# Kernel tuning notes

Measured on AMD Instinct MI355X. Metric: run time of the kernel, lower is better.

Reference implementation:

```python
import jax, jax.numpy as jnp
import numpy as np

B, T, E, D, A = 32, 2048, 1024, 1024, 1024
SHARPENING = 1.0


def setup_inputs() -> dict:
    key = jax.random.key(0)
    ks = jax.random.split(key, 8)
    s = 0.02
    return {
        "enc_out": jax.random.normal(ks[0], (B, T, E), jnp.float32),
        "x_lens": jax.random.randint(ks[1], (B,), 1, T + 1, jnp.int32),
        "dec_out": jax.random.normal(ks[2], (B, 1, D), jnp.float32),
        "att_weights_step": jax.random.uniform(ks[3], (B, T), jnp.float32),
        "W_enc": jax.random.normal(ks[4], (E, A), jnp.float32) * s,
        "b_enc": jnp.zeros((A,), jnp.float32),
        "W_dec": jax.random.normal(ks[5], (D, A), jnp.float32) * s,
        "v": jax.random.normal(ks[6], (A,), jnp.float32) * s,
    }


def reference(enc_out, x_lens, dec_out, att_weights_step, W_enc, b_enc, W_dec, v):
    # content (Bahdanau additive) attention
    # energy[b,t] = v . tanh(W_enc enc[b,t] + b_enc + W_dec dec[b])
    enc_proj = jnp.einsum("bte,ea->bta", enc_out, W_enc) + b_enc  # [B,T,A]
    dec_proj = jnp.einsum("bod,da->boa", dec_out, W_dec)          # [B,1,A]
    energy = jnp.einsum("bta,a->bt", jnp.tanh(enc_proj + dec_proj), v)  # [B,T]
    # original multiplies energy by a 0/1 length mask (NOT -inf masking)
    mask = (jnp.arange(T)[None, :] < x_lens[:, None]).astype(energy.dtype)
    energy = energy * mask * SHARPENING
    att = jax.nn.softmax(energy, axis=-1)  # [B,T]
    context_vec = jnp.einsum("bte,bt->be", enc_out, att)[:, None, :]  # [B,1,E]
    return context_vec, att
```

## Files before the change

### kernel.cpp

```cpp
#include <hip/hip_runtime.h>
#include <hip/hip_bf16.h>
#include <stdint.h>


typedef __bf16 bf16;
typedef __bf16 bf16x8 __attribute__((ext_vector_type(8)));
typedef __bf16 bf16x4 __attribute__((ext_vector_type(4)));
typedef float floatx4 __attribute__((ext_vector_type(4)));

#define T_DIM 2048
#define B_DIM 32
#define K_DIM 1024
#define N_DIM 1024
#define M_DIM (B_DIM * T_DIM)
#define ENC_ELEMS ((size_t)M_DIM * K_DIM)

__device__ __forceinline__ void async_copy16(const bf16* g, bf16* l) {
    __builtin_amdgcn_global_load_lds(
        (const __attribute__((address_space(1))) void*)g,
        (__attribute__((address_space(3))) void*)l, 16, 0, 0);
}

__device__ __forceinline__ float fast_tanh(float x) {
    float ax = fabsf(x);
    float e  = __expf(ax + ax);
    float t  = 1.f - 2.f / (e + 1.f);
    return copysignf(t, x);
}

__global__ __launch_bounds__(256) void cvt_enc(const float* __restrict__ in,
                                               bf16* __restrict__ out) {
    size_t i = ((size_t)blockIdx.x * 256 + threadIdx.x) * 8;
    const size_t stride = (size_t)gridDim.x * 256 * 8;
    for (; i < ENC_ELEMS; i += stride) {
        float4 f0 = *(const float4*)(in + i);
        float4 f1 = *(const float4*)(in + i + 4);
        bf16x8 w;
        w[0] = (bf16)f0.x; w[1] = (bf16)f0.y; w[2] = (bf16)f0.z; w[3] = (bf16)f0.w;
        w[4] = (bf16)f1.x; w[5] = (bf16)f1.y; w[6] = (bf16)f1.z; w[7] = (bf16)f1.w;
        *(bf16x8*)(out + i) = w;
    }
}

__global__ __launch_bounds__(256) void transpose_wenc(
        const float* __restrict__ W, bf16* __restrict__ WT) {
    __shared__ bf16 tile[64][65];
    const int e0 = blockIdx.x * 64, a0 = blockIdx.y * 64;
    const int c = threadIdx.x & 63, r0 = threadIdx.x >> 6;
#pragma unroll
    for (int p = 0; p < 16; ++p) {
        int r = p * 4 + r0;
        tile[r][c] = (bf16)W[(size_t)(e0 + r) * 1024 + a0 + c];
    }
    __syncthreads();
#pragma unroll
    for (int p = 0; p < 16; ++p) {
        int r = p * 4 + r0;
        WT[(size_t)(a0 + r) * 1024 + e0 + c] = tile[c][r];
    }
}

__global__ __launch_bounds__(256) void decproj_kernel(
        const float* __restrict__ dec, const float* __restrict__ Wdec,
        const float* __restrict__ benc, float* __restrict__ dproj) {
    const int bg = blockIdx.x;
    const int a0 = blockIdx.y * 64;
    const int al = threadIdx.x & 63;
    const int dq = threadIdx.x >> 6;
    const int a  = a0 + al;
    __shared__ float sdec[8][1024];
    for (int i = threadIdx.x; i < 8192; i += 256)
        sdec[i >> 10][i & 1023] = dec[bg * 8192 + i];
    __syncthreads();
    float acc[8];
#pragma unroll
    for (int b = 0; b < 8; ++b) acc[b] = 0.f;
    for (int d = dq * 256; d < dq * 256 + 256; ++d) {
        const float w = Wdec[(size_t)d * 1024 + a];
#pragma unroll
        for (int b = 0; b < 8; ++b) acc[b] += sdec[b][d] * w;
    }
    __shared__ float red[4][8][64];
#pragma unroll
    for (int b = 0; b < 8; ++b) red[dq][b][al] = acc[b];
    __syncthreads();
    if (dq == 0) {
        const float be = benc[a];
#pragma unroll
        for (int b = 0; b < 8; ++b)
            dproj[(bg * 8 + b) * 1024 + a] =
                be + red[0][b][al] + red[1][b][al] + red[2][b][al] + red[3][b][al];
    }
}


#define HT 8192

#define BARRIER()  __builtin_amdgcn_s_barrier()
#define SCHEDB()   __builtin_amdgcn_sched_barrier(0)
#define VMCNT(n)   asm volatile("s_waitcnt vmcnt(" #n ")")

#define STAGE_A(kt, h) {                                                       \
    const bf16* g_ = encb + (size_t)(m0 + (h)*128 + wave*8 + (lane>>3)) * 1024 \
                     + (kt)*64 + srccol;                                       \
    bf16* l_ = As + ((((kt)&1)*2 + (h)) * HT) + wave * 512;                    \
    async_copy16(g_, l_);                                                      \
    async_copy16(g_ + (size_t)64*1024, l_ + 4096);                             \
}
#define STAGE_B(kt, h) {                                                       \
    const bf16* g_ = WT + (size_t)(n0 + (h)*128 + wave*8 + (lane>>3)) * 1024   \
                     + (kt)*64 + srccol;                                       \
    bf16* l_ = Bs + ((((kt)&1)*2 + (h)) * HT) + wave * 512;                    \
    async_copy16(g_, l_);                                                      \
    async_copy16(g_ + (size_t)64*1024, l_ + 4096);                             \
}

#define PHASE(tt, qm, qn, RA, STAGECODE, WAITCODE) {                           \
    const bf16* Ah_ = As + (((tt) & 1) * 2 + (qm)) * HT;                       \
    const bf16* Bh_ = Bs + (((tt) & 1) * 2 + (qn)) * HT;                       \
    if (RA) {                                                                  \
      _Pragma("unroll") for (int mf_ = 0; mf_ < 4; ++mf_) {                    \
        afr[mf_][0] = *(const bf16x8*)(Ah_ + (wm*64 + mf_*16 + lo)*64 + swz0); \
        afr[mf_][1] = *(const bf16x8*)(Ah_ + (wm*64 + mf_*16 + lo)*64 + swz1); \
      }                                                                        \
    }                                                                          \
    _Pragma("unroll") for (int nf_ = 0; nf_ < 2; ++nf_) {                      \
      bfr[nf_][0] = *(const bf16x8*)(Bh_ + (wn*32 + nf_*16 + lo)*64 + swz0);   \
      bfr[nf_][1] = *(const bf16x8*)(Bh_ + (wn*32 + nf_*16 + lo)*64 + swz1);   \
    }                                                                          \
    STAGECODE;                                                                 \
    SCHEDB();                                                                  \
    BARRIER();                                                                 \
    SCHEDB();                                                                  \
    __builtin_amdgcn_s_setprio(1);                                             \
    _Pragma("unroll") for (int kk_ = 0; kk_ < 2; ++kk_)                        \
      _Pragma("unroll") for (int mf_ = 0; mf_ < 4; ++mf_)                      \
        _Pragma("unroll") for (int nf_ = 0; nf_ < 2; ++nf_)                    \
          acc[qm][qn][mf_][nf_] = __builtin_amdgcn_mfma_f32_16x16x32_bf16(     \
              afr[mf_][kk_], bfr[nf_][kk_], acc[qm][qn][mf_][nf_], 0, 0, 0);   \
    __builtin_amdgcn_s_setprio(0);                                             \
    SCHEDB();                                                                  \
    WAITCODE;                                                                  \
    SCHEDB();                                                                  \
    BARRIER();                                                                 \
    SCHEDB();                                                                  \
}

__global__ __launch_bounds__(512, 2) void energy_gemm_8ph(
        const bf16* __restrict__ encb, const bf16* __restrict__ WT,
        const float* __restrict__ dproj, const float* __restrict__ v,
        float* __restrict__ part) {
    __shared__ __align__(16) bf16 As[4 * HT];
    __shared__ __align__(16) bf16 Bs[4 * HT];
    __shared__ float esum[4 * 256];

    const int tid  = threadIdx.x;
    const int lane = tid & 63;
    const int wave = tid >> 6;
    const int wm   = wave >> 2;
    const int wn   = wave & 3;
    const int lo   = lane & 15;
    const int hi   = lane >> 4;

    const int L = blockIdx.x;
    const int xcd  = L & 7;
    const int slot = L >> 3;
    const int m_tile  = xcd * 32 + (slot >> 2);
    const int n_chunk = slot & 3;
    const int m0 = m_tile * 256;
    const int n0 = n_chunk * 256;
    const int b  = m0 >> 11;

    const int srccol = (((lane & 7) ^ (lane >> 3)) << 3);
    const int swz0 = ((hi)     ^ (lo & 7)) << 3;
    const int swz1 = ((4 | hi) ^ (lo & 7)) << 3;

    floatx4 acc[2][2][4][2];
#pragma unroll
    for (int a_ = 0; a_ < 2; ++a_)
#pragma unroll
      for (int b_ = 0; b_ < 2; ++b_)
#pragma unroll
        for (int c_ = 0; c_ < 4; ++c_)
#pragma unroll
          for (int d_ = 0; d_ < 2; ++d_)
            acc[a_][b_][c_][d_] = (floatx4){0.f, 0.f, 0.f, 0.f};

    bf16x8 afr[4][2], bfr[2][2];

    float vv[2][2], dp[2][2];
#pragma unroll
    for (int qn = 0; qn < 2; ++qn)
#pragma unroll
      for (int nf = 0; nf < 2; ++nf) {
        int col = n0 + qn * 128 + wn * 32 + nf * 16 + lo;
        vv[qn][nf] = v[col];
        dp[qn][nf] = dproj[b * 1024 + col];
      }
    SCHEDB();
    VMCNT(0);
    SCHEDB();

    STAGE_A(0, 0); STAGE_B(0, 0); STAGE_A(0, 1); STAGE_B(0, 1);
    STAGE_A(1, 0); STAGE_B(1, 0);
    SCHEDB();
    VMCNT(4);
    SCHEDB();
    BARRIER();
    SCHEDB();

#pragma unroll 1
    for (int i = 0; i < 7; ++i) {
        const int t0 = 2 * i, t1 = t0 + 1, t2 = t0 + 2, t3 = t0 + 3;
        PHASE(t0, 0, 0, 1, { STAGE_A(t1, 1); }, {});
        PHASE(t0, 0, 1, 0, { STAGE_B(t1, 1); }, {});
        PHASE(t0, 1, 0, 1, { STAGE_A(t2, 0); }, {});
        PHASE(t0, 1, 1, 0, { STAGE_B(t2, 0); }, { VMCNT(4); });
        PHASE(t1, 0, 0, 1, { STAGE_A(t2, 1); }, {});
        PHASE(t1, 0, 1, 0, { STAGE_B(t2, 1); }, {});
        PHASE(t1, 1, 0, 1, { STAGE_A(t3, 0); }, {});
        PHASE(t1, 1, 1, 0, { STAGE_B(t3, 0); }, { VMCNT(4); });
    }
    PHASE(14, 0, 0, 1, { STAGE_A(15, 1); }, {});
    PHASE(14, 0, 1, 0, { STAGE_B(15, 1); }, {});
    PHASE(14, 1, 0, 1, {}, {});
    PHASE(14, 1, 1, 0, {}, { VMCNT(0); });
    PHASE(15, 0, 0, 1, {}, {});
    PHASE(15, 0, 1, 0, {}, {});
    PHASE(15, 1, 0, 1, {}, {});
    PHASE(15, 1, 1, 0, {}, {});

#pragma unroll
    for (int qm = 0; qm < 2; ++qm)
#pragma unroll
      for (int mf = 0; mf < 4; ++mf)
#pragma unroll
        for (int r = 0; r < 4; ++r) {
          float s = 0.f;
#pragma unroll
          for (int qn = 0; qn < 2; ++qn)
#pragma unroll
            for (int nf = 0; nf < 2; ++nf)
              s += vv[qn][nf] * fast_tanh(acc[qm][qn][mf][nf][r] + dp[qn][nf]);
          s += __shfl_xor(s, 1);
          s += __shfl_xor(s, 2);
          s += __shfl_xor(s, 4);
          s += __shfl_xor(s, 8);
          if (lo == 0)
            esum[wn * 256 + qm * 128 + wm * 64 + mf * 16 + hi * 4 + r] = s;
        }
    __syncthreads();
    if (tid < 256)
        part[(size_t)n_chunk * M_DIM + m0 + tid] =
            esum[tid] + esum[256 + tid] + esum[512 + tid] + esum[768 + tid];
}

__global__ __launch_bounds__(256) void energy_gemm_f32(
        const float* __restrict__ enc, const bf16* __restrict__ WT,
        const float* __restrict__ dproj, const float* __restrict__ v,
        float* __restrict__ part) {
    __shared__ __align__(16) bf16 As[128 * 32];
    __shared__ __align__(16) bf16 Bs[128 * 32];
    __shared__ float esum[128];

    const int tid  = threadIdx.x;
    const int lane = tid & 63;
    const int wave = tid >> 6;
    const int wy = wave >> 1, wx = wave & 1;
    const int L = blockIdx.x;
    const int xcd  = L & 7;
    const int slot = L >> 3;
    const int m_tile = xcd * 64 + (slot >> 3);
    const int n_chunk = slot & 7;
    const int m0 = m_tile * 128;
    const int n0 = n_chunk * 128;
    const int b  = m0 >> 11;

    if (tid < 128) esum[tid] = 0.f;

    floatx4 acc[4][4];
#pragma unroll
    for (int i = 0; i < 4; ++i)
#pragma unroll
        for (int j = 0; j < 4; ++j) acc[i][j] = (floatx4){0.f, 0.f, 0.f, 0.f};

    const int sr = tid >> 2;
    const int sc = (tid & 3) * 8;
    const float* gA = enc + (size_t)(m0 + sr) * 1024 + sc;
    const bf16*  gB = WT  + (size_t)(n0 + sr) * 1024 + sc;
    bf16* lA = As + sr * 32 + sc;
    bf16* lB = Bs + sr * 32 + sc;

    for (int k0 = 0; k0 < K_DIM; k0 += 32) {
        __syncthreads();
#pragma unroll
        for (int rep = 0; rep < 2; ++rep) {
            const float4* p = (const float4*)(gA + (size_t)rep * 64 * 1024 + k0);
            float4 f0 = p[0], f1 = p[1];
            bf16x8 w;
            w[0] = (bf16)f0.x; w[1] = (bf16)f0.y; w[2] = (bf16)f0.z; w[3] = (bf16)f0.w;
            w[4] = (bf16)f1.x; w[5] = (bf16)f1.y; w[6] = (bf16)f1.z; w[7] = (bf16)f1.w;
            *(bf16x8*)(lA + rep * 64 * 32) = w;
            *(bf16x8*)(lB + rep * 64 * 32) =
                *(const bf16x8*)(gB + (size_t)rep * 64 * 1024 + k0);
        }
        __syncthreads();

        bf16x8 af[4], bfrg[4];
#pragma unroll
        for (int i = 0; i < 4; ++i)
            af[i] = *(const bf16x8*)(As + (wy * 64 + i * 16 + (lane & 15)) * 32 + (lane >> 4) * 8);
#pragma unroll
        for (int i = 0; i < 4; ++i)
            bfrg[i] = *(const bf16x8*)(Bs + (wx * 64 + i * 16 + (lane & 15)) * 32 + (lane >> 4) * 8);
#pragma unroll
        for (int mi = 0; mi < 4; ++mi)
#pragma unroll
            for (int ni = 0; ni < 4; ++ni)
                acc[mi][ni] = __builtin_amdgcn_mfma_f32_16x16x32_bf16(
                    af[mi], bfrg[ni], acc[mi][ni], 0, 0, 0);
    }
    __syncthreads();

    float vv[4], dp[4];
#pragma unroll
    for (int ni = 0; ni < 4; ++ni) {
        int col = n0 + wx * 64 + ni * 16 + (lane & 15);
        vv[ni] = v[col];
        dp[ni] = dproj[b * 1024 + col];
    }
#pragma unroll
    for (int mi = 0; mi < 4; ++mi) {
#pragma unroll
        for (int r = 0; r < 4; ++r) {
            float s = 0.f;
#pragma unroll
            for (int ni = 0; ni < 4; ++ni)
                s += vv[ni] * fast_tanh(acc[mi][ni][r] + dp[ni]);
            s += __shfl_xor(s, 1);
            s += __shfl_xor(s, 2);
            s += __shfl_xor(s, 4);
            s += __shfl_xor(s, 8);
            if ((lane & 15) == 0) {
                int row = wy * 64 + mi * 16 + (lane >> 4) * 4 + r;
                atomicAdd(&esum[row], s);
            }
        }
    }
    __syncthreads();
    if (tid < 128) part[(size_t)n_chunk * M_DIM + m0 + tid] = esum[tid];
}

__global__ __launch_bounds__(256) void softmax_kernel(
        const float* __restrict__ part, const int* __restrict__ xlens,
        float* __restrict__ att, int nc) {
    const int b = blockIdx.x, tid = threadIdx.x;
    const int len = xlens[b];
    float e[8];
    float mx = -3.4e38f;
#pragma unroll
    for (int i = 0; i < 8; ++i) {
        const int t = tid + i * 256;
        float s = 0.f;
#pragma unroll 4
        for (int c = 0; c < nc; ++c) s += part[(size_t)c * M_DIM + b * 2048 + t];
        e[i] = (t < len) ? s : 0.f;
        mx = fmaxf(mx, e[i]);
    }
#pragma unroll
    for (int off = 1; off < 64; off <<= 1) mx = fmaxf(mx, __shfl_xor(mx, off));
    __shared__ float sr1[4], sr2[4];
    if ((tid & 63) == 0) sr1[tid >> 6] = mx;
    __syncthreads();
    mx = fmaxf(fmaxf(sr1[0], sr1[1]), fmaxf(sr1[2], sr1[3]));
    float sum = 0.f;
#pragma unroll
    for (int i = 0; i < 8; ++i) { e[i] = __expf(e[i] - mx); sum += e[i]; }
#pragma unroll
    for (int off = 1; off < 64; off <<= 1) sum += __shfl_xor(sum, off);
    if ((tid & 63) == 0) sr2[tid >> 6] = sum;
    __syncthreads();
    sum = sr2[0] + sr2[1] + sr2[2] + sr2[3];
    const float inv = 1.f / sum;
#pragma unroll
    for (int i = 0; i < 8; ++i)
        att[b * 2048 + tid + i * 256] = e[i] * inv;
}

__global__ __launch_bounds__(256) void context_part_kernel(
        const bf16* __restrict__ encb, const float* __restrict__ att,
        float* __restrict__ ctxpart) {
    const int b = blockIdx.x, chunk = blockIdx.y, tid = threadIdx.x;
    const int t0 = chunk * 128;
    __shared__ float satt[128];
    if (tid < 128) satt[tid] = att[b * 2048 + t0 + tid];
    __syncthreads();
    const bf16* base = encb + ((size_t)b * 2048 + t0) * 1024 + tid * 4;
    float a0 = 0.f, a1 = 0.f, a2 = 0.f, a3 = 0.f;
#pragma unroll 4
    for (int t = 0; t < 128; ++t) {
        bf16x4 ev = *(const bf16x4*)(base + (size_t)t * 1024);
        float w = satt[t];
        a0 += w * (float)ev[0]; a1 += w * (float)ev[1];
        a2 += w * (float)ev[2]; a3 += w * (float)ev[3];
    }
    float* o = ctxpart + ((size_t)b * 16 + chunk) * 1024 + tid * 4;
    o[0] = a0; o[1] = a1; o[2] = a2; o[3] = a3;
}

__global__ __launch_bounds__(256) void context_reduce_kernel(
        const float* __restrict__ ctxpart, float* __restrict__ out_ctx) {
    const int i = blockIdx.x * 256 + threadIdx.x;
    const int b = i >> 10, e = i & 1023;
    const float* p = ctxpart + (size_t)b * 16 * 1024 + e;
    float s = 0.f;
#pragma unroll
    for (int c = 0; c < 16; ++c) s += p[c * 1024];
    out_ctx[i] = s;
}

__global__ __launch_bounds__(256) void context_kernel_f32(
        const float* __restrict__ enc, const float* __restrict__ att,
        float* __restrict__ ctx) {
    const int b = blockIdx.x, t0 = blockIdx.y * 128, tid = threadIdx.x;
    __shared__ float satt[128];
    if (tid < 128) satt[tid] = att[b * 2048 + t0 + tid];
    __syncthreads();
    const float* base = enc + ((size_t)b * 2048 + t0) * 1024 + tid * 4;
    float a0 = 0.f, a1 = 0.f, a2 = 0.f, a3 = 0.f;
    for (int t = 0; t < 128; ++t) {
        float4 ev = *(const float4*)(base + (size_t)t * 1024);
        float w = satt[t];
        a0 += w * ev.x; a1 += w * ev.y; a2 += w * ev.z; a3 += w * ev.w;
    }
    float* o = ctx + b * 1024 + tid * 4;
    atomicAdd(o + 0, a0); atomicAdd(o + 1, a1);
    atomicAdd(o + 2, a2); atomicAdd(o + 3, a3);
}

extern "C" void kernel_launch(void* const* d_in, const int* in_sizes, int n_in,
                              void* d_out, int out_size, void* d_ws, size_t ws_size,
                              hipStream_t stream) {
    const float* enc   = (const float*)d_in[0];
    const int*   xlens = (const int*)d_in[1];
    const float* dec   = (const float*)d_in[2];
    const float* Wenc  = (const float*)d_in[4];
    const float* benc  = (const float*)d_in[5];
    const float* Wdec  = (const float*)d_in[6];
    const float* v     = (const float*)d_in[7];

    float* out_ctx = (float*)d_out;
    float* out_att = out_ctx + B_DIM * K_DIM;

    char* ws = (char*)d_ws;
    float* dproj   = (float*)ws;
    bf16*  WT      = (bf16*)(ws + (128u << 10));
    float* part    = (float*)(ws + (128u << 10) + (2u << 20));
    bf16*  encb    = (bf16*)(ws + (128u << 10) + (4u << 20));
    float* ctxpart = (float*)(ws + (128u << 10) + (4u << 20) + (ENC_ELEMS * 2));
    const size_t need = (128u << 10) + (4u << 20) + ENC_ELEMS * 2 + (2u << 21);

    transpose_wenc<<<dim3(16, 16), 256, 0, stream>>>(Wenc, WT);
    decproj_kernel<<<dim3(4, 16), 256, 0, stream>>>(dec, Wdec, benc, dproj);

    if (ws_size >= need) {
        cvt_enc<<<2048, 256, 0, stream>>>(enc, encb);
        energy_gemm_8ph<<<1024, 512, 0, stream>>>(encb, WT, dproj, v, part);
        softmax_kernel<<<B_DIM, 256, 0, stream>>>(part, xlens, out_att, 4);
        context_part_kernel<<<dim3(B_DIM, 16), 256, 0, stream>>>(encb, out_att, ctxpart);
        context_reduce_kernel<<<B_DIM * K_DIM / 256, 256, 0, stream>>>(ctxpart, out_ctx);
    } else {
        hipMemsetAsync(out_ctx, 0, B_DIM * K_DIM * sizeof(float), stream);
        energy_gemm_f32<<<4096, 256, 0, stream>>>(enc, WT, dproj, v, part);
        softmax_kernel<<<B_DIM, 256, 0, stream>>>(part, xlens, out_att, 8);
        context_kernel_f32<<<dim3(B_DIM, 16), 256, 0, stream>>>(enc, out_att, out_ctx);
    }
}
```

Baseline: 621.2 us.

## Triple-buffer A tiles in LDS and restructure GEMM k-loop pipeline

The energy GEMM's A (encoder) tiles move from a 2-slot to a 3-slot LDS ring, so A is prefetched two k-steps ahead while B stays double-buffered one step ahead. The k-loop becomes a single rolled loop with a rotating slot index and conditional staging and waits, replacing the unrolled two-step body. The esum reduction buffer now aliases the A buffer, behind an added __syncthreads, to offset the extra LDS. The intent is to hide more of the global-to-LDS latency of the large A stream, at the cost of more LDS per block (risking the two-blocks-per-CU occupancy) and runtime-indexed slot addressing and branches inside the loop.

```diff
diff --git a/kernel.cpp b/kernel.cpp
--- a/kernel.cpp
+++ b/kernel.cpp
@@ -100,10 +100,10 @@
 #define SCHEDB()   __builtin_amdgcn_sched_barrier(0)
 #define VMCNT(n)   asm volatile("s_waitcnt vmcnt(" #n ")")
 
-#define STAGE_A(kt, h) {                                                       \
+#define STAGE_A(kt, h, sl) {                                                   \
     const bf16* g_ = encb + (size_t)(m0 + (h)*128 + wave*8 + (lane>>3)) * 1024 \
                      + (kt)*64 + srccol;                                       \
-    bf16* l_ = As + ((((kt)&1)*2 + (h)) * HT) + wave * 512;                    \
+    bf16* l_ = As + (((sl)*2 + (h)) * HT) + wave * 512;                        \
     async_copy16(g_, l_);                                                      \
     async_copy16(g_ + (size_t)64*1024, l_ + 4096);                             \
 }
@@ -115,9 +115,9 @@
     async_copy16(g_ + (size_t)64*1024, l_ + 4096);                             \
 }
 
-#define PHASE(tt, qm, qn, RA, STAGECODE, WAITCODE) {                           \
-    const bf16* Ah_ = As + (((tt) & 1) * 2 + (qm)) * HT;                       \
-    const bf16* Bh_ = Bs + (((tt) & 1) * 2 + (qn)) * HT;                       \
+#define PHASE(asl, tb, qm, qn, RA, STAGECODE, WAITCODE) {                      \
+    const bf16* Ah_ = As + ((asl) * 2 + (qm)) * HT;                            \
+    const bf16* Bh_ = Bs + ((tb) * 2 + (qn)) * HT;                             \
     if (RA) {                                                                  \
       _Pragma("unroll") for (int mf_ = 0; mf_ < 4; ++mf_) {                    \
         afr[mf_][0] = *(const bf16x8*)(Ah_ + (wm*64 + mf_*16 + lo)*64 + swz0); \
@@ -150,9 +150,9 @@
         const bf16* __restrict__ encb, const bf16* __restrict__ WT,
         const float* __restrict__ dproj, const float* __restrict__ v,
         float* __restrict__ part) {
-    __shared__ __align__(16) bf16 As[4 * HT];
+    __shared__ __align__(16) bf16 As[6 * HT];
     __shared__ __align__(16) bf16 Bs[4 * HT];
-    __shared__ float esum[4 * 256];
+    float* esum = (float*)As;
 
     const int tid  = threadIdx.x;
     const int lane = tid & 63;
@@ -201,35 +201,29 @@
     VMCNT(0);
     SCHEDB();
 
-    STAGE_A(0, 0); STAGE_B(0, 0); STAGE_A(0, 1); STAGE_B(0, 1);
-    STAGE_A(1, 0); STAGE_B(1, 0);
+    STAGE_B(0, 0); STAGE_B(0, 1);
+    STAGE_A(0, 0, 0); STAGE_A(0, 1, 0);
+    STAGE_A(1, 0, 1); STAGE_A(1, 1, 1);
     SCHEDB();
     VMCNT(4);
     SCHEDB();
     BARRIER();
     SCHEDB();
 
+    int aslot = 0;
 #pragma unroll 1
-    for (int i = 0; i < 7; ++i) {
-        const int t0 = 2 * i, t1 = t0 + 1, t2 = t0 + 2, t3 = t0 + 3;
-        PHASE(t0, 0, 0, 1, { STAGE_A(t1, 1); }, {});
-        PHASE(t0, 0, 1, 0, { STAGE_B(t1, 1); }, {});
-        PHASE(t0, 1, 0, 1, { STAGE_A(t2, 0); }, {});
-        PHASE(t0, 1, 1, 0, { STAGE_B(t2, 0); }, { VMCNT(4); });
-        PHASE(t1, 0, 0, 1, { STAGE_A(t2, 1); }, {});
-        PHASE(t1, 0, 1, 0, { STAGE_B(t2, 1); }, {});
-        PHASE(t1, 1, 0, 1, { STAGE_A(t3, 0); }, {});
-        PHASE(t1, 1, 1, 0, { STAGE_B(t3, 0); }, { VMCNT(4); });
-    }
-    PHASE(14, 0, 0, 1, { STAGE_A(15, 1); }, {});
-    PHASE(14, 0, 1, 0, { STAGE_B(15, 1); }, {});
-    PHASE(14, 1, 0, 1, {}, {});
-    PHASE(14, 1, 1, 0, {}, { VMCNT(0); });
-    PHASE(15, 0, 0, 1, {}, {});
-    PHASE(15, 0, 1, 0, {}, {});
-    PHASE(15, 1, 0, 1, {}, {});
-    PHASE(15, 1, 1, 0, {}, {});
-
+    for (int t = 0; t < 16; ++t) {
+        const int tb   = t & 1;
+        const int asl2 = (aslot >= 1) ? (aslot - 1) : 2;
+        PHASE(aslot, tb, 0, 0, 1, { if (t < 15) STAGE_B(t + 1, 0); }, {});
+        PHASE(aslot, tb, 0, 1, 0, { if (t < 15) STAGE_B(t + 1, 1); }, {});
+        PHASE(aslot, tb, 1, 0, 1, { if (t < 14) STAGE_A(t + 2, 0, asl2); }, {});
+        PHASE(aslot, tb, 1, 1, 0, { if (t < 14) STAGE_A(t + 2, 1, asl2); },
+              { if (t < 14) { VMCNT(4); } else if (t == 14) { VMCNT(0); } });
+        aslot = (aslot == 2) ? 0 : aslot + 1;
+    }
+
+    __syncthreads();
 #pragma unroll
     for (int qm = 0; qm < 2; ++qm)
 #pragma unroll
```

Measured after the change: 613.5 us. No clear change (-1.2%).
